# Kernel optimization log

Measured on AMD Instinct MI355X. Metric: run time of the kernel, lower is better.

Reference implementation:

```python
import jax, jax.numpy as jnp
import numpy as np

B, T, D, U = 32, 512, 1024, 1024
EPS = 1e-08


def setup_inputs() -> dict:
    key = jax.random.key(0)
    k1, k2, k3 = jax.random.split(key, 3)
    # scale weights for numerical sanity (glorot/orthogonal-ish magnitudes)
    kernel = jax.random.normal(k1, (D, 4 * U), dtype=jnp.float32) * (1.0 / np.sqrt(D))
    recurrent_kernel = jax.random.normal(k2, (U, 4 * U), dtype=jnp.float32) * (1.0 / np.sqrt(U))
    bias = jnp.zeros((4 * U,), dtype=jnp.float32)
    x = jax.random.normal(k3, (B, T, D), dtype=jnp.float32)
    return {"x": x, "kernel": kernel, "recurrent_kernel": recurrent_kernel, "bias": bias}


def reference(x, kernel, recurrent_kernel, bias):
    """sLSTM (xLSTM Sec 2.2) with sigmoid forget gate + log/exp/max stabilization,
    scanned over the time axis. Returns h of shape (B, T, U)."""
    U_ = bias.shape[0] // 4
    Bsz = x.shape[0]
    # precompute input projections for all timesteps: (T, B, 4U)
    x_proj = jnp.einsum('btd,dg->tbg', x, kernel) + bias

    def step(carry, xp_t):
        h, c, n, m = carry
        proj = xp_t + h @ recurrent_kernel          # (B, 4U)
        i_p, f_p, o_p, z_p = jnp.split(proj, 4, axis=-1)
        log_f = jnp.log(jax.nn.sigmoid(f_p) + EPS)
        m_t = jnp.maximum(m + log_f, i_p)
        i_t = jnp.exp(i_p - m_t)
        f_t = jnp.exp(m + log_f - m_t)
        o_t = jax.nn.sigmoid(o_p)
        z_t = jnp.tanh(z_p)
        c_t = f_t * c + i_t * z_t
        n_t = f_t * n + i_t
        h_t = o_t * (c_t / (n_t + EPS))
        return (h_t, c_t, n_t, m_t), h_t

    zeros = jnp.zeros((Bsz, U_), dtype=x.dtype)
    init = (zeros, zeros, zeros, zeros)
    _, hs = jax.lax.scan(step, init, x_proj)        # hs: (T, B, U)
    return jnp.transpose(hs, (1, 0, 2))             # (B, T, U)
```

## Files before the change

### kernel.cpp

```cpp
#include <hip/hip_runtime.h>

typedef unsigned short u16;
typedef short short8 __attribute__((ext_vector_type(8)));
typedef float f32x4 __attribute__((ext_vector_type(4)));
typedef unsigned int u32x4 __attribute__((ext_vector_type(4)));
typedef unsigned short u16x4 __attribute__((ext_vector_type(4)));

#define Bsz 32
#define Tsz 512
#define Dsz 1024
#define Usz 1024
#define Gsz 4096

static __device__ __forceinline__ u16 f2bf(float f) {
    unsigned int u = __float_as_uint(f);
    unsigned int lsb = (u >> 16) & 1u;
    u += 0x7fffu + lsb;
    return (u16)(u >> 16);
}
static __device__ __forceinline__ float bf2f(u16 b) {
    return __uint_as_float(((unsigned int)b) << 16);
}


__global__ __launch_bounds__(256) void pack_a(const float* __restrict__ x, u16* __restrict__ Af) {
    size_t tid = (size_t)blockIdx.x * 256 + threadIdx.x;
    int L = (int)(tid & 63);
    size_t mtkb = tid >> 6;
    int kb = (int)(mtkb & 31);
    int mt = (int)(mtkb >> 5);
    int m  = mt * 16 + (L & 15);
    int d0 = kb * 32 + (L >> 4) * 8;
    const float* src = x + (size_t)m * Dsz + d0;
    short8 v;
#pragma unroll
    for (int j = 0; j < 8; ++j) v[j] = (short)f2bf(src[j]);
    *(short8*)(Af + tid * 8) = v;
}

__global__ __launch_bounds__(256) void pack_b(const float* __restrict__ W, u16* __restrict__ Bf) {
    size_t tid = (size_t)blockIdx.x * 256 + threadIdx.x;
    int L = (int)(tid & 63);
    size_t ntkb = tid >> 6;
    int kb = (int)(ntkb & 31);
    int nt = (int)(ntkb >> 5);
    int n  = nt * 16 + (L & 15);
    int k0 = kb * 32 + (L >> 4) * 8;
    short8 v;
#pragma unroll
    for (int j = 0; j < 8; ++j) v[j] = (short)f2bf(W[(size_t)(k0 + j) * Gsz + n]);
    *(short8*)(Bf + tid * 8) = v;
}

__global__ __launch_bounds__(256) void pack_r(const float* __restrict__ R, u16* __restrict__ Rp,
                                              unsigned* __restrict__ flags) {
    if (blockIdx.x == 0) flags[threadIdx.x] = 0;
    size_t tid = (size_t)blockIdx.x * 256 + threadIdx.x;
    int L = (int)(tid & 63);
    size_t bkkb = tid >> 6;
    int kb  = (int)(bkkb & 31);
    int blk = (int)(bkkb >> 5);
    int c = L & 15;
    int gate = c >> 2, du = c & 3;
    int g = gate * 1024 + blk * 4 + du;
    int k0 = kb * 32 + (L >> 4) * 8;
    short8 v;
#pragma unroll
    for (int j = 0; j < 8; ++j) v[j] = (short)f2bf(R[(size_t)(k0 + j) * Gsz + g]);
    *(short8*)(Rp + tid * 8) = v;
}

__global__ __launch_bounds__(256) void gemm1(const u16* __restrict__ Af, const u16* __restrict__ Bf,
                                             float* __restrict__ xpf, u16* __restrict__ xph, int xp32) {
    __shared__ u16 smem[16 * 512];
    int bm = blockIdx.x >> 5;
    int bn = blockIdx.x & 31;
    int tid = threadIdx.x;
    int w = tid >> 6, ln = tid & 63;
    int mw = w & 1, nw = w >> 1;

    f32x4 acc[4][4];
#pragma unroll
    for (int i = 0; i < 4; ++i)
#pragma unroll
        for (int j = 0; j < 4; ++j) acc[i][j] = (f32x4){0.f, 0.f, 0.f, 0.f};

    for (int kb = 0; kb < 32; ++kb) {
        short8 tmp[4];
#pragma unroll
        for (int c2 = 0; c2 < 4; ++c2) {
            int chunk = w * 4 + c2;
            const u16* src = (chunk < 8)
                ? Af + (((size_t)(bm * 8 + chunk) * 32 + kb) * 64 + ln) * 8
                : Bf + (((size_t)(bn * 8 + (chunk - 8)) * 32 + kb) * 64 + ln) * 8;
            tmp[c2] = *(const short8*)src;
        }
#pragma unroll
        for (int c2 = 0; c2 < 4; ++c2) {
            int chunk = w * 4 + c2;
            *(short8*)(smem + chunk * 512 + ln * 8) = tmp[c2];
        }
        __syncthreads();
        short8 av[4], bv[4];
#pragma unroll
        for (int i = 0; i < 4; ++i) av[i] = *(const short8*)(smem + (mw * 4 + i) * 512 + ln * 8);
#pragma unroll
        for (int j = 0; j < 4; ++j) bv[j] = *(const short8*)(smem + (8 + nw * 4 + j) * 512 + ln * 8);
#pragma unroll
        for (int i = 0; i < 4; ++i)
#pragma unroll
            for (int j = 0; j < 4; ++j)
                acc[i][j] = __builtin_amdgcn_mfma_f32_16x16x32_bf16(av[i], bv[j], acc[i][j], 0, 0, 0);
        __syncthreads();
    }

    int quad = ln >> 4, c15 = ln & 15;
#pragma unroll
    for (int i = 0; i < 4; ++i) {
        int mt_g = bm * 8 + mw * 4 + i;
#pragma unroll
        for (int j = 0; j < 4; ++j) {
            int g = (bn * 8 + nw * 4 + j) * 16 + c15;
            int p = ((g & 1023) >> 2) * 16 + (g & 3) * 4 + (g >> 10);
#pragma unroll
            for (int r = 0; r < 4; ++r) {
                int row = mt_g * 16 + quad * 4 + r;
                int bb = row >> 9, tt = row & 511;
                size_t o = ((size_t)tt * Bsz + bb) * Gsz + p;
                if (xp32) xpf[o] = acc[i][j][r];
                else      xph[o] = f2bf(acc[i][j][r]);
            }
        }
    }
}

__global__ __launch_bounds__(256) void scan_all(const float* __restrict__ xpf,
                                                const u16* __restrict__ xph, int xp32,
                                                const u16* __restrict__ Rp,
                                                const float* __restrict__ bias,
                                                u16* __restrict__ hbf, float* __restrict__ out,
                                                unsigned* __restrict__ flags) {
    __shared__ u16 lds_r[16384];
    __shared__ float partial[2][64][4];
    __shared__ float proj[32][17];

    int tid = threadIdx.x;
    int blk = blockIdx.x;
    int w = tid >> 6, ln = tid & 63, quad = ln >> 4, c15 = ln & 15;
    int mt = w & 1, kh = w >> 1;
    bool upd = (tid < 128);
    int b_row = tid >> 2, du = tid & 3;
    int u_g = blk * 4 + du;

    u16* hb0 = hbf;
    u16* hb1 = hbf + 32 * 1024;

    const u16* rsrc = Rp + (size_t)blk * 16384;
#pragma unroll
    for (int i = 0; i < 8; ++i)
        *(short8*)(lds_r + tid * 64 + i * 8) = *(const short8*)(rsrc + tid * 64 + i * 8);

    float bi[4] = {0.f, 0.f, 0.f, 0.f};
    float cs = 0.f, ns = 0.f, ms = 0.f;
    float xpn0 = 0.f, xpn1 = 0.f, xpn2 = 0.f, xpn3 = 0.f;

    if (upd) {
#pragma unroll
        for (int g = 0; g < 4; ++g) bi[g] = bias[g * 1024 + u_g];
        u16* hp = hb1 + b_row * Usz + u_g;
        unsigned z = 0;
        asm volatile("global_store_short %0, %1, off sc0 sc1" :: "v"(hp), "v"(z) : "memory");
        size_t o0 = ((size_t)0 * Bsz + b_row) * Gsz + blk * 16 + du * 4;
        if (xp32) { float4 v4 = *(const float4*)(xpf + o0); xpn0 = v4.x; xpn1 = v4.y; xpn2 = v4.z; xpn3 = v4.w; }
        else      { u16x4 v = *(const u16x4*)(xph + o0); xpn0 = bf2f(v[0]); xpn1 = bf2f(v[1]); xpn2 = bf2f(v[2]); xpn3 = bf2f(v[3]); }
    }
    asm volatile("s_waitcnt vmcnt(0)" ::: "memory");
    __syncthreads();
    if (tid == 0) {
        unsigned* fp = flags + blk;
        unsigned one = 1;
        asm volatile("global_store_dword %0, %1, off sc0 sc1" :: "v"(fp), "v"(one) : "memory");
    }

    const u16* aB0 = hb0 + (size_t)(mt * 16 + c15) * Usz + quad * 8 + kh * 512;
    const u16* aB1 = hb1 + (size_t)(mt * 16 + c15) * Usz + quad * 8 + kh * 512;

    for (int t = 0; t < Tsz; ++t) {
        if (w == 0) {
            const unsigned* fp4 = flags + ln * 4;
            unsigned tgt = (unsigned)(t + 1);
            u32x4 fv;
            do {
                asm volatile("global_load_dwordx4 %0, %1, off sc0 sc1\n\ts_waitcnt vmcnt(0)"
                             : "=v"(fv) : "v"(fp4) : "memory");
            } while (__any((int)(fv[0] < tgt || fv[1] < tgt || fv[2] < tgt || fv[3] < tgt)));
        }
        __syncthreads();

        float xv0 = xpn0, xv1 = xpn1, xv2 = xpn2, xv3 = xpn3;
        if (upd) {
            int tn = (t + 1 < Tsz) ? t + 1 : t;
            size_t o = ((size_t)tn * Bsz + b_row) * Gsz + blk * 16 + du * 4;
            if (xp32) { float4 v4 = *(const float4*)(xpf + o); xpn0 = v4.x; xpn1 = v4.y; xpn2 = v4.z; xpn3 = v4.w; }
            else      { u16x4 v = *(const u16x4*)(xph + o); xpn0 = bf2f(v[0]); xpn1 = bf2f(v[1]); xpn2 = bf2f(v[2]); xpn3 = bf2f(v[3]); }
        }

        const u16* aBw = (t & 1) ? aB0 : aB1;
        short8 av[16];
#define LDH(i, OFF) asm volatile("global_load_dwordx4 %0, %1, off offset:" OFF " sc0 sc1" \
                                 : "=v"(av[i]) : "v"(aBw))
        LDH(0, "0");   LDH(1, "64");  LDH(2, "128"); LDH(3, "192");
        LDH(4, "256"); LDH(5, "320"); LDH(6, "384"); LDH(7, "448");
        LDH(8, "512"); LDH(9, "576"); LDH(10, "640"); LDH(11, "704");
        LDH(12, "768"); LDH(13, "832"); LDH(14, "896"); LDH(15, "960");
#undef LDH
        asm volatile("s_waitcnt vmcnt(0)" ::: "memory");

        f32x4 acc0 = (f32x4){0.f, 0.f, 0.f, 0.f};
        f32x4 acc1 = (f32x4){0.f, 0.f, 0.f, 0.f};
#pragma unroll
        for (int kk = 0; kk < 16; kk += 2) {
            short8 b0 = *(const short8*)(lds_r + ((kh * 16 + kk) * 64 + ln) * 8);
            short8 b1 = *(const short8*)(lds_r + ((kh * 16 + kk + 1) * 64 + ln) * 8);
            acc0 = __builtin_amdgcn_mfma_f32_16x16x32_bf16(av[kk], b0, acc0, 0, 0, 0);
            acc1 = __builtin_amdgcn_mfma_f32_16x16x32_bf16(av[kk + 1], b1, acc1, 0, 0, 0);
        }
        f32x4 acc = acc0 + acc1;

        if (w >= 2) *(f32x4*)(&partial[w - 2][ln][0]) = acc;
        __syncthreads();
        if (w < 2) {
            f32x4 p = *(const f32x4*)(&partial[w][ln][0]);
#pragma unroll
            for (int r = 0; r < 4; ++r) proj[mt * 16 + quad * 4 + r][c15] = acc[r] + p[r];
        }
        __syncthreads();

        if (upd) {
            float ip = proj[b_row][du]      + xv0 + bi[0];
            float fp = proj[b_row][4 + du]  + xv1 + bi[1];
            float op = proj[b_row][8 + du]  + xv2 + bi[2];
            float zp = proj[b_row][12 + du] + xv3 + bi[3];
            float sf = 1.f / (1.f + __expf(-fp));
            float lf = __logf(sf + 1e-8f);
            float mn = fmaxf(ms + lf, ip);
            float it = __expf(ip - mn);
            float ft = __expf(ms + lf - mn);
            float ot = 1.f / (1.f + __expf(-op));
            float zt = tanhf(zp);
            cs = ft * cs + it * zt;
            ns = ft * ns + it;
            ms = mn;
            float h = ot * (cs / (ns + 1e-8f));
            out[(size_t)b_row * (Tsz * Usz) + (size_t)t * Usz + u_g] = h;
            u16* hp = ((t & 1) ? hb1 : hb0) + b_row * Usz + u_g;
            unsigned hv = (unsigned)f2bf(h);
            asm volatile("global_store_short %0, %1, off sc0 sc1" :: "v"(hp), "v"(hv) : "memory");
        }
        asm volatile("s_waitcnt vmcnt(0)" ::: "memory");
        __syncthreads();
        if (tid == 0) {
            unsigned* fp = flags + blk;
            unsigned val = (unsigned)(t + 2);
            asm volatile("global_store_dword %0, %1, off sc0 sc1" :: "v"(fp), "v"(val) : "memory");
        }
    }
}

extern "C" void kernel_launch(void* const* d_in, const int* in_sizes, int n_in,
                              void* d_out, int out_size, void* d_ws, size_t ws_size,
                              hipStream_t stream) {
    const float* x    = (const float*)d_in[0];
    const float* W    = (const float*)d_in[1];
    const float* R    = (const float*)d_in[2];
    const float* bias = (const float*)d_in[3];
    float* out = (float*)d_out;

    char* ws = (char*)d_ws;
    size_t off = 0;
    u16* Af = (u16*)(ws + off); off += (size_t)16384 * 1024 * 2;
    u16* Bf = (u16*)(ws + off); off += (size_t)1024 * 4096 * 2;
    u16* Rp = (u16*)(ws + off); off += (size_t)1024 * 4096 * 2;
    u16* hbf = (u16*)(ws + off); off += (size_t)1 << 20;
    unsigned* flags = (unsigned*)(ws + off); off += 4096;
    size_t xp_need32 = (size_t)16384 * 4096 * 4;
    int xp32 = (ws_size >= off + xp_need32) ? 1 : 0;
    float* xpf = (float*)(ws + off);
    u16*   xph = (u16*)(ws + off);

    pack_a<<<dim3(8192), dim3(256), 0, stream>>>(x, Af);
    pack_b<<<dim3(2048), dim3(256), 0, stream>>>(W, Bf);
    pack_r<<<dim3(2048), dim3(256), 0, stream>>>(R, Rp, flags);
    gemm1<<<dim3(4096), dim3(256), 0, stream>>>(Af, Bf, xpf, xph, xp32);

    void* args[] = { (void*)&xpf, (void*)&xph, (void*)&xp32, (void*)&Rp,
                     (void*)&bias, (void*)&hbf, (void*)&out, (void*)&flags };
    hipLaunchCooperativeKernel((const void*)scan_all, dim3(256), dim3(256), args, 0, stream);
}
```

Before: 2.812 ms.

## Halve scan workgroups to 128, keep recurrent weights in registers, stage h via LDS

The recurrent scan now runs 128 workgroups of 512 threads, each owning 8 hidden units instead of 4. This halves the number of flags each step must poll and the number of cross-workgroup participants in the grid-wide barrier. Each wave keeps its slice of the recurrent weight matrix in registers. The full h vector is loaded cooperatively from global memory into LDS once per step rather than each wave loading its own copy, and h is written back as one vectorized store per batch row. The cost is higher register pressure from holding the weights, extra __syncthreads, and fewer CUs active on the serial recurrence.

```diff
diff --git a/kernel.cpp b/kernel.cpp
--- a/kernel.cpp
+++ b/kernel.cpp
@@ -3,7 +3,7 @@
 typedef unsigned short u16;
 typedef short short8 __attribute__((ext_vector_type(8)));
 typedef float f32x4 __attribute__((ext_vector_type(4)));
-typedef unsigned int u32x4 __attribute__((ext_vector_type(4)));
+typedef unsigned int u32x2 __attribute__((ext_vector_type(2)));
 typedef unsigned short u16x4 __attribute__((ext_vector_type(4)));
 
 #define Bsz 32
@@ -57,12 +57,12 @@
     if (blockIdx.x == 0) flags[threadIdx.x] = 0;
     size_t tid = (size_t)blockIdx.x * 256 + threadIdx.x;
     int L = (int)(tid & 63);
-    size_t bkkb = tid >> 6;
-    int kb  = (int)(bkkb & 31);
-    int blk = (int)(bkkb >> 5);
-    int c = L & 15;
-    int gate = c >> 2, du = c & 3;
-    int g = gate * 1024 + blk * 4 + du;
+    int kb = (int)((tid >> 6) & 31);
+    int tt = (int)(tid >> 11);
+    int blk = tt >> 1, nt = tt & 1;
+    int cc = nt * 16 + (L & 15);
+    int gate = cc >> 3, du = cc & 7;
+    int g = gate * 1024 + blk * 8 + du;
     int k0 = kb * 32 + (L >> 4) * 8;
     short8 v;
 #pragma unroll
@@ -121,7 +121,7 @@
 #pragma unroll
         for (int j = 0; j < 4; ++j) {
             int g = (bn * 8 + nw * 4 + j) * 16 + c15;
-            int p = ((g & 1023) >> 2) * 16 + (g & 3) * 4 + (g >> 10);
+            int p = ((g & 1023) >> 3) * 32 + (g & 7) * 4 + (g >> 10);
 #pragma unroll
             for (int r = 0; r < 4; ++r) {
                 int row = mt_g * 16 + quad * 4 + r;
@@ -134,45 +134,44 @@
     }
 }
 
-__global__ __launch_bounds__(256) void scan_all(const float* __restrict__ xpf,
+__global__ __launch_bounds__(512) void scan_all(const float* __restrict__ xpf,
                                                 const u16* __restrict__ xph, int xp32,
                                                 const u16* __restrict__ Rp,
                                                 const float* __restrict__ bias,
                                                 u16* __restrict__ hbf, float* __restrict__ out,
                                                 unsigned* __restrict__ flags) {
-    __shared__ u16 lds_r[16384];
-    __shared__ float partial[2][64][4];
-    __shared__ float proj[32][17];
+    __shared__ u16 hlds[64 * 64 * 8];
+    __shared__ float partial[4][64][4];
+    __shared__ float proj[32][34];
+    __shared__ u16 hstage[32][8];
 
     int tid = threadIdx.x;
     int blk = blockIdx.x;
     int w = tid >> 6, ln = tid & 63, quad = ln >> 4, c15 = ln & 15;
-    int mt = w & 1, kh = w >> 1;
-    bool upd = (tid < 128);
-    int b_row = tid >> 2, du = tid & 3;
-    int u_g = blk * 4 + du;
+    int mt = w & 1, nt = (w >> 1) & 1, kh = w >> 2;
+    bool upd = (tid < 256);
+    int b_row = tid >> 3, du = tid & 7;
+    int u_g = blk * 8 + du;
 
     u16* hb0 = hbf;
     u16* hb1 = hbf + 32 * 1024;
 
-    const u16* rsrc = Rp + (size_t)blk * 16384;
-#pragma unroll
-    for (int i = 0; i < 8; ++i)
-        *(short8*)(lds_r + tid * 64 + i * 8) = *(const short8*)(rsrc + tid * 64 + i * 8);
+    short8 bfr[16];
+    {
+        const u16* bB = Rp + (((size_t)(blk * 2 + nt) * 32 + kh * 16) * 64 + ln) * 8;
+#pragma unroll
+        for (int kk = 0; kk < 16; ++kk)
+            bfr[kk] = *(const short8*)(bB + (size_t)kk * 512);
+    }
 
     float bi[4] = {0.f, 0.f, 0.f, 0.f};
     float cs = 0.f, ns = 0.f, ms = 0.f;
-    float xpn0 = 0.f, xpn1 = 0.f, xpn2 = 0.f, xpn3 = 0.f;
-
     if (upd) {
 #pragma unroll
         for (int g = 0; g < 4; ++g) bi[g] = bias[g * 1024 + u_g];
         u16* hp = hb1 + b_row * Usz + u_g;
         unsigned z = 0;
         asm volatile("global_store_short %0, %1, off sc0 sc1" :: "v"(hp), "v"(z) : "memory");
-        size_t o0 = ((size_t)0 * Bsz + b_row) * Gsz + blk * 16 + du * 4;
-        if (xp32) { float4 v4 = *(const float4*)(xpf + o0); xpn0 = v4.x; xpn1 = v4.y; xpn2 = v4.z; xpn3 = v4.w; }
-        else      { u16x4 v = *(const u16x4*)(xph + o0); xpn0 = bf2f(v[0]); xpn1 = bf2f(v[1]); xpn2 = bf2f(v[2]); xpn3 = bf2f(v[3]); }
     }
     asm volatile("s_waitcnt vmcnt(0)" ::: "memory");
     __syncthreads();
@@ -182,88 +181,99 @@
         asm volatile("global_store_dword %0, %1, off sc0 sc1" :: "v"(fp), "v"(one) : "memory");
     }
 
-    const u16* aB0 = hb0 + (size_t)(mt * 16 + c15) * Usz + quad * 8 + kh * 512;
-    const u16* aB1 = hb1 + (size_t)(mt * 16 + c15) * Usz + quad * 8 + kh * 512;
-
     for (int t = 0; t < Tsz; ++t) {
         if (w == 0) {
-            const unsigned* fp4 = flags + ln * 4;
+            const unsigned* fp2 = flags + ln * 2;
             unsigned tgt = (unsigned)(t + 1);
-            u32x4 fv;
+            u32x2 fv;
             do {
-                asm volatile("global_load_dwordx4 %0, %1, off sc0 sc1\n\ts_waitcnt vmcnt(0)"
-                             : "=v"(fv) : "v"(fp4) : "memory");
-            } while (__any((int)(fv[0] < tgt || fv[1] < tgt || fv[2] < tgt || fv[3] < tgt)));
-        }
-        __syncthreads();
-
-        float xv0 = xpn0, xv1 = xpn1, xv2 = xpn2, xv3 = xpn3;
+                asm volatile("global_load_dwordx2 %0, %1, off sc0 sc1\n\ts_waitcnt vmcnt(0)"
+                             : "=v"(fv) : "v"(fp2) : "memory");
+            } while (__any((int)(fv[0] < tgt || fv[1] < tgt)));
+        }
+        __syncthreads();
+
+        const u16* rb = (t & 1) ? hb0 : hb1;
+        short8 st[8];
+#pragma unroll
+        for (int it = 0; it < 8; ++it) {
+            int f = it * 8 + w;
+            int m = (f >> 5) * 16 + (ln & 15);
+            int u0 = (f & 31) * 32 + ((ln >> 4) & 3) * 8;
+            const u16* gp = rb + m * Usz + u0;
+            asm volatile("global_load_dwordx4 %0, %1, off sc0 sc1" : "=v"(st[it]) : "v"(gp));
+        }
+        float xv0 = 0.f, xv1 = 0.f, xv2 = 0.f, xv3 = 0.f;
         if (upd) {
-            int tn = (t + 1 < Tsz) ? t + 1 : t;
-            size_t o = ((size_t)tn * Bsz + b_row) * Gsz + blk * 16 + du * 4;
-            if (xp32) { float4 v4 = *(const float4*)(xpf + o); xpn0 = v4.x; xpn1 = v4.y; xpn2 = v4.z; xpn3 = v4.w; }
-            else      { u16x4 v = *(const u16x4*)(xph + o); xpn0 = bf2f(v[0]); xpn1 = bf2f(v[1]); xpn2 = bf2f(v[2]); xpn3 = bf2f(v[3]); }
-        }
-
-        const u16* aBw = (t & 1) ? aB0 : aB1;
-        short8 av[16];
-#define LDH(i, OFF) asm volatile("global_load_dwordx4 %0, %1, off offset:" OFF " sc0 sc1" \
-                                 : "=v"(av[i]) : "v"(aBw))
-        LDH(0, "0");   LDH(1, "64");  LDH(2, "128"); LDH(3, "192");
-        LDH(4, "256"); LDH(5, "320"); LDH(6, "384"); LDH(7, "448");
-        LDH(8, "512"); LDH(9, "576"); LDH(10, "640"); LDH(11, "704");
-        LDH(12, "768"); LDH(13, "832"); LDH(14, "896"); LDH(15, "960");
-#undef LDH
+            size_t o = ((size_t)t * Bsz + b_row) * Gsz + blk * 32 + du * 4;
+            if (xp32) { float4 v4 = *(const float4*)(xpf + o); xv0 = v4.x; xv1 = v4.y; xv2 = v4.z; xv3 = v4.w; }
+            else      { u16x4 v = *(const u16x4*)(xph + o); xv0 = bf2f(v[0]); xv1 = bf2f(v[1]); xv2 = bf2f(v[2]); xv3 = bf2f(v[3]); }
+        }
         asm volatile("s_waitcnt vmcnt(0)" ::: "memory");
+#pragma unroll
+        for (int it = 0; it < 8; ++it) {
+            int f = it * 8 + w;
+            *(short8*)(hlds + ((size_t)f * 64 + ln) * 8) = st[it];
+        }
+        __syncthreads();
 
         f32x4 acc0 = (f32x4){0.f, 0.f, 0.f, 0.f};
         f32x4 acc1 = (f32x4){0.f, 0.f, 0.f, 0.f};
 #pragma unroll
         for (int kk = 0; kk < 16; kk += 2) {
-            short8 b0 = *(const short8*)(lds_r + ((kh * 16 + kk) * 64 + ln) * 8);
-            short8 b1 = *(const short8*)(lds_r + ((kh * 16 + kk + 1) * 64 + ln) * 8);
-            acc0 = __builtin_amdgcn_mfma_f32_16x16x32_bf16(av[kk], b0, acc0, 0, 0, 0);
-            acc1 = __builtin_amdgcn_mfma_f32_16x16x32_bf16(av[kk + 1], b1, acc1, 0, 0, 0);
+            short8 a0 = *(const short8*)(hlds + (((mt * 32 + kh * 16 + kk) * 64) + ln) * 8);
+            short8 a1 = *(const short8*)(hlds + (((mt * 32 + kh * 16 + kk + 1) * 64) + ln) * 8);
+            acc0 = __builtin_amdgcn_mfma_f32_16x16x32_bf16(a0, bfr[kk], acc0, 0, 0, 0);
+            acc1 = __builtin_amdgcn_mfma_f32_16x16x32_bf16(a1, bfr[kk + 1], acc1, 0, 0, 0);
         }
         f32x4 acc = acc0 + acc1;
 
-        if (w >= 2) *(f32x4*)(&partial[w - 2][ln][0]) = acc;
-        __syncthreads();
-        if (w < 2) {
+        if (kh == 1) *(f32x4*)(&partial[w - 4][ln][0]) = acc;
+        __syncthreads();
+        if (kh == 0) {
             f32x4 p = *(const f32x4*)(&partial[w][ln][0]);
 #pragma unroll
-            for (int r = 0; r < 4; ++r) proj[mt * 16 + quad * 4 + r][c15] = acc[r] + p[r];
-        }
-        __syncthreads();
-
+            for (int r = 0; r < 4; ++r)
+                proj[mt * 16 + quad * 4 + r][nt * 16 + c15] = acc[r] + p[r];
+        }
+        __syncthreads();
+
+        float h = 0.f;
         if (upd) {
             float ip = proj[b_row][du]      + xv0 + bi[0];
-            float fp = proj[b_row][4 + du]  + xv1 + bi[1];
-            float op = proj[b_row][8 + du]  + xv2 + bi[2];
-            float zp = proj[b_row][12 + du] + xv3 + bi[3];
+            float fp = proj[b_row][8 + du]  + xv1 + bi[1];
+            float op = proj[b_row][16 + du] + xv2 + bi[2];
+            float zp = proj[b_row][24 + du] + xv3 + bi[3];
             float sf = 1.f / (1.f + __expf(-fp));
             float lf = __logf(sf + 1e-8f);
             float mn = fmaxf(ms + lf, ip);
-            float it = __expf(ip - mn);
+            float it_ = __expf(ip - mn);
             float ft = __expf(ms + lf - mn);
             float ot = 1.f / (1.f + __expf(-op));
             float zt = tanhf(zp);
-            cs = ft * cs + it * zt;
-            ns = ft * ns + it;
+            cs = ft * cs + it_ * zt;
+            ns = ft * ns + it_;
             ms = mn;
-            float h = ot * (cs / (ns + 1e-8f));
+            h = ot * (cs / (ns + 1e-8f));
+            hstage[b_row][du] = f2bf(h);
+        }
+        __syncthreads();
+
+        if (w == 0) {
+            if (ln < 32) {
+                short8 hv = *(const short8*)(&hstage[ln][0]);
+                u16* hp = ((t & 1) ? hb1 : hb0) + ln * Usz + blk * 8;
+                asm volatile("global_store_dwordx4 %0, %1, off sc0 sc1" :: "v"(hp), "v"(hv) : "memory");
+            }
+            asm volatile("s_waitcnt vmcnt(0)" ::: "memory");
+            if (ln == 0) {
+                unsigned* fp = flags + blk;
+                unsigned val = (unsigned)(t + 2);
+                asm volatile("global_store_dword %0, %1, off sc0 sc1" :: "v"(fp), "v"(val) : "memory");
+            }
+        }
+        if (upd)
             out[(size_t)b_row * (Tsz * Usz) + (size_t)t * Usz + u_g] = h;
-            u16* hp = ((t & 1) ? hb1 : hb0) + b_row * Usz + u_g;
-            unsigned hv = (unsigned)f2bf(h);
-            asm volatile("global_store_short %0, %1, off sc0 sc1" :: "v"(hp), "v"(hv) : "memory");
-        }
-        asm volatile("s_waitcnt vmcnt(0)" ::: "memory");
-        __syncthreads();
-        if (tid == 0) {
-            unsigned* fp = flags + blk;
-            unsigned val = (unsigned)(t + 2);
-            asm volatile("global_store_dword %0, %1, off sc0 sc1" :: "v"(fp), "v"(val) : "memory");
-        }
     }
 }
 
@@ -295,5 +305,5 @@
 
     void* args[] = { (void*)&xpf, (void*)&xph, (void*)&xp32, (void*)&Rp,
                      (void*)&bias, (void*)&hbf, (void*)&out, (void*)&flags };
-    hipLaunchCooperativeKernel((const void*)scan_all, dim3(256), dim3(256), args, 0, stream);
-}
+    hipLaunchCooperativeKernel((const void*)scan_all, dim3(128), dim3(512), args, 0, stream);
+}
```

Measured after the change: 3.743 ms. +33.1%, slower.
